# Performance work log

Hardware: AMD Instinct MI355X
Metric: run time of the kernel (lower is better)

## Reference

```python
import jax, jax.numpy as jnp
import numpy as np

B, T, N = 512, 512, 128   # batch, timesteps, driving series
M = 64                    # LSTM hidden size
UNITS = 64                # attention units


def setup_inputs() -> dict:
    key = jax.random.key(0)
    ks = jax.random.split(key, 9)
    s = lambda fan_in: 1.0 / np.sqrt(fan_in)
    return {
        "x": jax.random.normal(ks[0], (B, T, N), jnp.float32),
        "hidden_state": jax.random.normal(ks[1], (B, M), jnp.float32),
        "cell_state": jax.random.normal(ks[2], (B, M), jnp.float32),
        # Dense(units) applied to x permuted to (B, N, T): kernel contracts T
        "w1_kernel": jax.random.normal(ks[3], (T, UNITS), jnp.float32) * s(T),
        "w1_bias": jnp.zeros((UNITS,), jnp.float32),
        # Dense(units) applied to query (B, N, 2M)
        "w2_kernel": jax.random.normal(ks[4], (2 * M, UNITS), jnp.float32) * s(2 * M),
        "w2_bias": jnp.zeros((UNITS,), jnp.float32),
        # Dense(1) scoring
        "v_kernel": jax.random.normal(ks[5], (UNITS, 1), jnp.float32) * s(UNITS),
        "v_bias": jnp.zeros((1,), jnp.float32),
    }


def reference(x, hidden_state, cell_state, w1_kernel, w1_bias,
              w2_kernel, w2_bias, v_kernel, v_bias):
    # query: (B, 2M) -> broadcast over the N feature axis (RepeatVector)
    query = jnp.concatenate([hidden_state, cell_state], axis=-1)
    q_proj = query @ w2_kernel + w2_bias                    # (B, UNITS)
    x_perm = jnp.transpose(x, (0, 2, 1))                    # (B, N, T)
    score = jnp.tanh(x_perm @ w1_kernel + w1_bias + q_proj[:, None, :])  # (B, N, UNITS)
    score = score @ v_kernel + v_bias                       # (B, N, 1)
    score = jnp.transpose(score, (0, 2, 1))                 # (B, 1, N)
    attention_weights = jax.nn.softmax(score, axis=-1)      # (B, 1, N)
    context_vector = jnp.sum(attention_weights * x, axis=-1)  # (B, T)
    return context_vector, attention_weights
```

## Files before the change

### kernel.cpp

```cpp
#include <hip/hip_runtime.h>
#include <hip/hip_bf16.h>

namespace {

constexpr int kB = 512, kT = 512, kN = 128, kM = 64, kU = 64;

typedef __attribute__((ext_vector_type(8))) short short8;
typedef __attribute__((ext_vector_type(16))) float f32x16;

__device__ __forceinline__ float fb16(unsigned h) { return __uint_as_float(h << 16); }

union FragU { unsigned u[4]; uint4 q; short8 s; };

__device__ __forceinline__ unsigned bc2(__hip_bfloat162 v) {
  union { __hip_bfloat162 b; unsigned u; } c; c.b = v; return c.u;
}

__device__ __forceinline__ void pack8(const float* v, short8& hi, short8& lo) {
  FragU H, L;
#pragma unroll
  for (int jj = 0; jj < 4; ++jj) {
    float v0 = v[2 * jj], v1 = v[2 * jj + 1];
    __hip_bfloat162 h2 = __float22bfloat162_rn(float2{v0, v1});
    float h0 = __bfloat162float(h2.x), h1 = __bfloat162float(h2.y);
    __hip_bfloat162 l2 = __float22bfloat162_rn(float2{v0 - h0, v1 - h1});
    H.u[jj] = bc2(h2);
    L.u[jj] = bc2(l2);
  }
  hi = H.s; lo = L.s;
}

__device__ __forceinline__ float fast_tanh(float x) {
  return 1.0f - 2.0f / (__expf(2.0f * x) + 1.0f);
}

struct Smem {
  float qpart[4][kU];
  float qpfull[kU];
  float sn[kN];
  float aw[kN];
};

__global__ __launch_bounds__(256) void prep_w1(const float* __restrict__ w1,
                                               unsigned* __restrict__ pwh,
                                               unsigned* __restrict__ pwl) {
  const int gid = blockIdx.x * blockDim.x + threadIdx.x;
  const int j = gid & 3, u = (gid >> 2) & 63, tg = gid >> 8;
  const int t = tg * 8 + 2 * j;
  float v0 = w1[t * kU + u], v1 = w1[(t + 1) * kU + u];
  __hip_bfloat162 h2 = __float22bfloat162_rn(float2{v0, v1});
  float h0 = __bfloat162float(h2.x), h1 = __bfloat162float(h2.y);
  __hip_bfloat162 l2 = __float22bfloat162_rn(float2{v0 - h0, v1 - h1});
  pwh[gid] = bc2(h2);
  pwl[gid] = bc2(l2);
}

__global__ __launch_bounds__(256, 4) void fused_kernel(
    const float* __restrict__ x,
    const float* __restrict__ hs,
    const float* __restrict__ cs,
    const unsigned* __restrict__ pwh,
    const unsigned* __restrict__ pwl,
    const float* __restrict__ w1b,
    const float* __restrict__ w2,
    const float* __restrict__ w2b,
    const float* __restrict__ vk,
    float* __restrict__ ctx_out,
    float* __restrict__ aw_out)
{
  __shared__ Smem s;

  const int b = blockIdx.x;
  const int tid = threadIdx.x;
  const int l = tid & 63;
  const int w = tid >> 6;
  const int ln = l & 31;
  const int kh = l >> 5;
  const int nA = 32 * w + ln;

  {
    const int u = tid & 63, kg = tid >> 6;
    float a0 = 0.f;
#pragma unroll
    for (int j = 0; j < 32; ++j) {
      int k = kg * 32 + j;
      float qv = (k < kM) ? hs[(size_t)b * kM + k] : cs[(size_t)b * kM + (k - kM)];
      a0 = fmaf(qv, w2[k * kU + u], a0);
    }
    s.qpart[kg][u] = a0;
  }

  f32x16 acc0, acc1;
#pragma unroll
  for (int i = 0; i < 16; ++i) { acc0[i] = 0.f; acc1[i] = 0.f; }

  const float* xb = x + (size_t)b * kT * kN;

  struct SubBuf { float rA[2][8]; uint4 rbh[2][2]; uint4 rbl[2][2]; };

  auto issue = [&](SubBuf& bf, int sub) {
    const int tb = sub * 32;
#pragma unroll
    for (int ks = 0; ks < 2; ++ks) {
      const int t0 = tb + ks * 16 + 8 * kh;
#pragma unroll
      for (int j = 0; j < 8; ++j)
        bf.rA[ks][j] = xb[(size_t)(t0 + j) * kN + nA];
#pragma unroll
      for (int ut = 0; ut < 2; ++ut) {
        const int base = ((t0 >> 3) * 64 + 32 * ut + ln) * 4;
        bf.rbh[ks][ut] = *(const uint4*)&pwh[base];
        bf.rbl[ks][ut] = *(const uint4*)&pwl[base];
      }
    }
  };

  auto compute = [&](SubBuf& bf) {
#pragma unroll
    for (int ks = 0; ks < 2; ++ks) {
      short8 ah, al;
      pack8(bf.rA[ks], ah, al);
#pragma unroll
      for (int ut = 0; ut < 2; ++ut) {
        FragU BH, BL;
        BH.q = bf.rbh[ks][ut];
        BL.q = bf.rbl[ks][ut];
        f32x16& a = ut ? acc1 : acc0;
        a = __builtin_amdgcn_mfma_f32_32x32x16_bf16(ah, BH.s, a, 0, 0, 0);
        a = __builtin_amdgcn_mfma_f32_32x32x16_bf16(ah, BL.s, a, 0, 0, 0);
        a = __builtin_amdgcn_mfma_f32_32x32x16_bf16(al, BH.s, a, 0, 0, 0);
      }
    }
  };

  {
    SubBuf A_, B_;
    issue(A_, 0);
    issue(B_, 1);
#pragma unroll
    for (int s2 = 0; s2 < 16; s2 += 2) {
      compute(A_);
      if (s2 + 2 < 16) issue(A_, s2 + 2);
      compute(B_);
      if (s2 + 3 < 16) issue(B_, s2 + 3);
    }
  }

  __syncthreads();

  if (tid < kU) {
    float v = w2b[tid] + w1b[tid];
#pragma unroll
    for (int gg = 0; gg < 4; ++gg) v += s.qpart[gg][tid];
    s.qpfull[tid] = v;
  }
  __syncthreads();

  {
    const float qp0 = s.qpfull[ln], qp1 = s.qpfull[32 + ln];
    const float v0 = vk[ln], v1 = vk[32 + ln];
    float pr[16];
#pragma unroll
    for (int r = 0; r < 16; ++r)
      pr[r] = fmaf(fast_tanh(acc0[r] + qp0), v0, fast_tanh(acc1[r] + qp1) * v1);
#pragma unroll
    for (int off = 1; off < 32; off <<= 1)
#pragma unroll
      for (int r = 0; r < 16; ++r)
        pr[r] += __shfl_xor(pr[r], off);
    if (ln == 0) {
#pragma unroll
      for (int r = 0; r < 16; ++r)
        s.sn[32 * w + (r & 3) + 8 * (r >> 2) + 4 * kh] = pr[r];
    }
  }
  __syncthreads();

  if (tid < 64) {
    float s0 = s.sn[tid], s1 = s.sn[tid + 64];
    float mx = fmaxf(s0, s1);
#pragma unroll
    for (int off = 32; off > 0; off >>= 1) mx = fmaxf(mx, __shfl_xor(mx, off));
    float e0 = __expf(s0 - mx), e1 = __expf(s1 - mx);
    float se = e0 + e1;
#pragma unroll
    for (int off = 32; off > 0; off >>= 1) se += __shfl_xor(se, off);
    float inv = 1.0f / se;
    float a0 = e0 * inv, a1 = e1 * inv;
    s.aw[tid] = a0;
    s.aw[tid + 64] = a1;
    aw_out[(size_t)b * kN + tid] = a0;
    aw_out[(size_t)b * kN + tid + 64] = a1;
  }
  __syncthreads();

  {
    const float4 av = *(const float4*)&s.aw[4 * ln];
    const int tbase = 128 * w;
    float o0 = 0.f, o1 = 0.f;
#pragma unroll 8
    for (int r = 0; r < 32; ++r) {
      const int t = tbase + 2 * r + kh;
      float4 v = *(const float4*)&xb[(size_t)t * kN + 4 * ln];
      float p = fmaf(v.x, av.x, fmaf(v.y, av.y, fmaf(v.z, av.z, v.w * av.w)));
#pragma unroll
      for (int off = 1; off < 32; off <<= 1) p += __shfl_xor(p, off);
      if (ln == r) o0 = p;
    }
#pragma unroll 8
    for (int r = 0; r < 32; ++r) {
      const int t = tbase + 64 + 2 * r + kh;
      float4 v = *(const float4*)&xb[(size_t)t * kN + 4 * ln];
      float p = fmaf(v.x, av.x, fmaf(v.y, av.y, fmaf(v.z, av.z, v.w * av.w)));
#pragma unroll
      for (int off = 1; off < 32; off <<= 1) p += __shfl_xor(p, off);
      if (ln == r) o1 = p;
    }
    ctx_out[(size_t)b * kT + tbase + 2 * ln + kh] = o0;
    ctx_out[(size_t)b * kT + tbase + 64 + 2 * ln + kh] = o1;
  }
}

}

extern "C" void kernel_launch(void* const* d_in, const int* in_sizes, int n_in,
                              void* d_out, int out_size, void* d_ws, size_t ws_size,
                              hipStream_t stream) {
  const float* x   = (const float*)d_in[0];
  const float* hs  = (const float*)d_in[1];
  const float* cs  = (const float*)d_in[2];
  const float* w1  = (const float*)d_in[3];
  const float* w1b = (const float*)d_in[4];
  const float* w2  = (const float*)d_in[5];
  const float* w2b = (const float*)d_in[6];
  const float* vk  = (const float*)d_in[7];

  float* out = (float*)d_out;
  float* ctx = out;
  float* awo = out + (size_t)kB * kT;

  unsigned* pwh = (unsigned*)d_ws;
  unsigned* pwl = (unsigned*)d_ws + 16384;

  hipLaunchKernelGGL(prep_w1, dim3(64), dim3(256), 0, stream, w1, pwh, pwl);
  hipLaunchKernelGGL(fused_kernel, dim3(kB), dim3(256), 0, stream,
                     x, hs, cs, pwh, pwl, w1b, w2, w2b, vk, ctx, awo);
}
```

Before: 226.9 us.

## Split T reduction across two wave groups with 512-thread blocks and LDS reduction

Doubles the block to 512 threads (8 waves): two groups of four waves each compute the x·W1 MFMA product over half of the T dimension, and the partial accumulators are then summed through shared memory. The query projection and the final context pass are likewise spread over 8 waves. The intent is to put more waves in flight per batch row so the memory-latency-bound streaming of x is hidden better. In exchange it adds an LDS reduction with extra barriers, about 18 KB more shared memory, and idles half the waves during the tanh/score stage.

```diff
diff --git a/kernel.cpp b/kernel.cpp
--- a/kernel.cpp
+++ b/kernel.cpp
@@ -4,11 +4,10 @@
 namespace {
 
 constexpr int kB = 512, kT = 512, kN = 128, kM = 64, kU = 64;
+constexpr int RST = 18;
 
 typedef __attribute__((ext_vector_type(8))) short short8;
 typedef __attribute__((ext_vector_type(16))) float f32x16;
-
-__device__ __forceinline__ float fb16(unsigned h) { return __uint_as_float(h << 16); }
 
 union FragU { unsigned u[4]; uint4 q; short8 s; };
 
@@ -35,7 +34,8 @@
 }
 
 struct Smem {
-  float qpart[4][kU];
+  float red[256 * RST];
+  float qpart[8][kU];
   float qpfull[kU];
   float sn[kN];
   float aw[kN];
@@ -55,7 +55,7 @@
   pwl[gid] = bc2(l2);
 }
 
-__global__ __launch_bounds__(256, 4) void fused_kernel(
+__global__ __launch_bounds__(512, 4) void fused_kernel(
     const float* __restrict__ x,
     const float* __restrict__ hs,
     const float* __restrict__ cs,
@@ -74,16 +74,18 @@
   const int tid = threadIdx.x;
   const int l = tid & 63;
   const int w = tid >> 6;
+  const int g = w >> 2;
+  const int m = w & 3;
   const int ln = l & 31;
   const int kh = l >> 5;
-  const int nA = 32 * w + ln;
+  const int nA = 32 * m + ln;
 
   {
     const int u = tid & 63, kg = tid >> 6;
     float a0 = 0.f;
 #pragma unroll
-    for (int j = 0; j < 32; ++j) {
-      int k = kg * 32 + j;
+    for (int j = 0; j < 16; ++j) {
+      int k = kg * 16 + j;
       float qv = (k < kM) ? hs[(size_t)b * kM + k] : cs[(size_t)b * kM + (k - kM)];
       a0 = fmaf(qv, w2[k * kU + u], a0);
     }
@@ -99,7 +101,7 @@
   struct SubBuf { float rA[2][8]; uint4 rbh[2][2]; uint4 rbl[2][2]; };
 
   auto issue = [&](SubBuf& bf, int sub) {
-    const int tb = sub * 32;
+    const int tb = g * 256 + sub * 32;
 #pragma unroll
     for (int ks = 0; ks < 2; ++ks) {
       const int t0 = tb + ks * 16 + 8 * kh;
@@ -138,25 +140,41 @@
     issue(A_, 0);
     issue(B_, 1);
 #pragma unroll
-    for (int s2 = 0; s2 < 16; s2 += 2) {
+    for (int s2 = 0; s2 < 8; s2 += 2) {
       compute(A_);
-      if (s2 + 2 < 16) issue(A_, s2 + 2);
+      if (s2 + 2 < 8) issue(A_, s2 + 2);
       compute(B_);
-      if (s2 + 3 < 16) issue(B_, s2 + 3);
-    }
-  }
-
-  __syncthreads();
+      if (s2 + 3 < 8) issue(B_, s2 + 3);
+    }
+  }
+
+  __syncthreads();
+
+  const int rrow = ((w & 3) * 64 + l) * RST;
+#pragma unroll
+  for (int rnd = 0; rnd < 2; ++rnd) {
+    f32x16& a = rnd ? acc1 : acc0;
+    if (g == 1) {
+#pragma unroll
+      for (int j = 0; j < 16; ++j) s.red[rrow + j] = a[j];
+    }
+    __syncthreads();
+    if (g == 0) {
+#pragma unroll
+      for (int j = 0; j < 16; ++j) a[j] += s.red[rrow + j];
+    }
+    __syncthreads();
+  }
 
   if (tid < kU) {
     float v = w2b[tid] + w1b[tid];
 #pragma unroll
-    for (int gg = 0; gg < 4; ++gg) v += s.qpart[gg][tid];
+    for (int gg = 0; gg < 8; ++gg) v += s.qpart[gg][tid];
     s.qpfull[tid] = v;
   }
   __syncthreads();
 
-  {
+  if (g == 0) {
     const float qp0 = s.qpfull[ln], qp1 = s.qpfull[32 + ln];
     const float v0 = vk[ln], v1 = vk[32 + ln];
     float pr[16];
@@ -171,7 +189,7 @@
     if (ln == 0) {
 #pragma unroll
       for (int r = 0; r < 16; ++r)
-        s.sn[32 * w + (r & 3) + 8 * (r >> 2) + 4 * kh] = pr[r];
+        s.sn[32 * m + (r & 3) + 8 * (r >> 2) + 4 * kh] = pr[r];
     }
   }
   __syncthreads();
@@ -196,8 +214,8 @@
 
   {
     const float4 av = *(const float4*)&s.aw[4 * ln];
-    const int tbase = 128 * w;
-    float o0 = 0.f, o1 = 0.f;
+    const int tbase = 64 * w;
+    float o0 = 0.f;
 #pragma unroll 8
     for (int r = 0; r < 32; ++r) {
       const int t = tbase + 2 * r + kh;
@@ -207,17 +225,7 @@
       for (int off = 1; off < 32; off <<= 1) p += __shfl_xor(p, off);
       if (ln == r) o0 = p;
     }
-#pragma unroll 8
-    for (int r = 0; r < 32; ++r) {
-      const int t = tbase + 64 + 2 * r + kh;
-      float4 v = *(const float4*)&xb[(size_t)t * kN + 4 * ln];
-      float p = fmaf(v.x, av.x, fmaf(v.y, av.y, fmaf(v.z, av.z, v.w * av.w)));
-#pragma unroll
-      for (int off = 1; off < 32; off <<= 1) p += __shfl_xor(p, off);
-      if (ln == r) o1 = p;
-    }
     ctx_out[(size_t)b * kT + tbase + 2 * ln + kh] = o0;
-    ctx_out[(size_t)b * kT + tbase + 64 + 2 * ln + kh] = o1;
   }
 }
 
@@ -243,6 +251,6 @@
   unsigned* pwl = (unsigned*)d_ws + 16384;
 
   hipLaunchKernelGGL(prep_w1, dim3(64), dim3(256), 0, stream, w1, pwh, pwl);
-  hipLaunchKernelGGL(fused_kernel, dim3(kB), dim3(256), 0, stream,
+  hipLaunchKernelGGL(fused_kernel, dim3(kB), dim3(512), 0, stream,
                      x, hs, cs, pwh, pwl, w1b, w2, w2b, vk, ctx, awo);
 }
```

After: 228.8 us. Within noise of the previous version (+0.9%).
